# Performance work log

Hardware: AMD Instinct MI355X
Metric: run time of the kernel (lower is better)

The kernel has to match this reference:

```python
import jax, jax.numpy as jnp
import numpy as np

D = 2048      # in_features (model dim)
H = 1408      # d_intermediate (hidden per expert)
E = 16        # n_routed_experts
T = 16384     # flattened tokens
K = 4         # top_k experts per token


def setup_inputs() -> dict:
    key = jax.random.key(0)
    k1, k2, k3, k4, k5 = jax.random.split(key, 5)
    x = jax.random.normal(k1, (T, D), dtype=jnp.float32)
    weights = jax.random.uniform(k2, (T, K), dtype=jnp.float32)
    indices = jax.random.randint(k3, (T, K), 0, E)
    # Stacked GatedMLP params (bias=False as in mamba's GatedMLP):
    # fc1: [2H, D] per expert, fc2: [D, H] per expert
    W1 = jax.random.normal(k4, (E, 2 * H, D), dtype=jnp.float32) * (D ** -0.5)
    W2 = jax.random.normal(k5, (E, D, H), dtype=jnp.float32) * (H ** -0.5)
    return {"x": x, "weights": weights, "indices": indices, "W1": W1, "W2": W2}


def reference(x, weights, indices, W1, W2):
    # y[t] = sum_i ( GatedMLP_i(x[t]) * sum_k weights[t,k] * [indices[t,k]==i] )
    n_experts = W1.shape[0]
    y = jnp.zeros_like(x)
    for i in range(n_experts):  # small fixed expert loop
        # combined routing weight of expert i per token (handles duplicate hits like += in torch)
        cw = jnp.sum(weights * (indices == i), axis=-1)      # [T]
        h = x @ W1[i].T                                      # [T, 2H]
        u, g = jnp.split(h, 2, axis=-1)                      # chunk(2, dim=-1): (y, gate)
        out = (u * jax.nn.silu(g)) @ W2[i].T                 # [T, D]
        y = y + out * cw[:, None]
    return y
```

## Files before the change

kernel.cpp:

```cpp
#include <hip/hip_runtime.h>

#define D_ 2048
#define H_ 1408
#define E_ 16
#define T_ 16384
#define K_ 4
#define TK_ 65536
#define BM_ 256
#define BK_ 64
#define MAXT_ 272
#define CVTB_ 408

typedef __attribute__((ext_vector_type(8))) short bf16x8;
typedef __attribute__((ext_vector_type(4))) float f32x4;
typedef __attribute__((ext_vector_type(4))) unsigned short u16x4;

#define M_NT     49
#define M_TE     64
#define M_TR     (64 + MAXT_)
#define M_TN     (64 + 2*MAXT_)

#define XB_OFF   0ULL
#define W1B_OFF  67108864ULL
#define W2B_OFF  (W1B_OFF + 188743680ULL)
#define ACT_OFF  (W2B_OFF + 94371840ULL)
#define PERM_OFF (ACT_OFF + 184549376ULL)
#define WGT_OFF  (PERM_OFF + 262144ULL)
#define META_B   (WGT_OFF + 262144ULL)

#define SBAR()  __builtin_amdgcn_s_barrier()
#define SCHED() __builtin_amdgcn_sched_barrier(0)
#define LGK0()  asm volatile("s_waitcnt lgkmcnt(0)" ::: "memory")
#define LGK2()  asm volatile("s_waitcnt lgkmcnt(2)" ::: "memory")
#define LGK4()  asm volatile("s_waitcnt lgkmcnt(4)" ::: "memory")
#define LGK6()  asm volatile("s_waitcnt lgkmcnt(6)" ::: "memory")
#define VM6()   asm volatile("s_waitcnt vmcnt(6)" ::: "memory")
#define PRIO1() __builtin_amdgcn_s_setprio(1)
#define PRIO0() __builtin_amdgcn_s_setprio(0)

static __device__ __forceinline__ unsigned short f2bf(float f) {
  unsigned u = __builtin_bit_cast(unsigned, f);
  u += 0x7fffu + ((u >> 16) & 1u);
  return (unsigned short)(u >> 16);
}

static __device__ __forceinline__ void gload16(const void* g, unsigned ldsOff) {
  __builtin_amdgcn_global_load_lds(
      (const __attribute__((address_space(1))) unsigned int*)(unsigned long long)g,
      (__attribute__((address_space(3))) unsigned int*)(unsigned long long)ldsOff,
      16, 0, 0);
}

__global__ __launch_bounds__(1024) void prep_kernel(
    const float* __restrict__ x, const float* __restrict__ W1,
    const int* __restrict__ idx, const float* __restrict__ wts,
    float* __restrict__ y, unsigned short* __restrict__ xb,
    unsigned short* __restrict__ w1b, int* __restrict__ meta,
    int* __restrict__ perm, float* __restrict__ wgt) {
  const int tid = threadIdx.x;
  if (blockIdx.x == gridDim.x - 1) {
    __shared__ int cnt[E_], cur[E_];
    if (tid < E_) cnt[tid] = 0;
    __syncthreads();
    for (int i = tid; i < TK_; i += 1024) atomicAdd(&cnt[idx[i]], 1);
    __syncthreads();
    if (tid == 0) {
      int off = 0, nt = 0;
      for (int e = 0; e < E_; ++e) {
        cur[e] = off;
        const int c = cnt[e];
        for (int r = 0; r < c; r += BM_) {
          meta[M_TE + nt] = e;
          meta[M_TR + nt] = off + r;
          meta[M_TN + nt] = (c - r < BM_) ? (c - r) : BM_;
          ++nt;
        }
        off += c;
      }
      meta[M_NT] = nt;
    }
    __syncthreads();
    for (int i = tid; i < TK_; i += 1024) {
      const int pos = atomicAdd(&cur[idx[i]], 1);
      perm[pos] = i >> 2;
      wgt[pos] = wts[i];
    }
    return;
  }
  const long long base = ((long long)blockIdx.x * 1024 + tid) * 4;
  const long long stride = (long long)(gridDim.x - 1) * 1024 * 4;
  for (long long i = base; i < (long long)T_ * D_; i += stride)
    *reinterpret_cast<float4*>(y + i) = (float4){0.f, 0.f, 0.f, 0.f};
  for (long long i = base; i < (long long)T_ * D_; i += stride) {
    float4 v = *reinterpret_cast<const float4*>(x + i);
    u16x4 o = { f2bf(v.x), f2bf(v.y), f2bf(v.z), f2bf(v.w) };
    *reinterpret_cast<u16x4*>(xb + i) = o;
  }
  for (long long i = base; i < (long long)E_ * 2 * H_ * D_; i += stride) {
    float4 v = *reinterpret_cast<const float4*>(W1 + i);
    u16x4 o = { f2bf(v.x), f2bf(v.y), f2bf(v.z), f2bf(v.w) };
    *reinterpret_cast<u16x4*>(w1b + i) = o;
  }
}

__global__ __launch_bounds__(512, 2) void gemm1_kernel(
    const char* __restrict__ xb, const char* __restrict__ w1b,
    const int* __restrict__ perm, const int* __restrict__ meta,
    unsigned short* __restrict__ act,
    const float* __restrict__ W2, unsigned short* __restrict__ w2b) {
  const int tid = threadIdx.x;
  const int bid0 = (int)blockIdx.x;
  if (bid0 < CVTB_) {
    long long i = ((long long)bid0 * 512 + tid) * 4;
    const long long stride = (long long)CVTB_ * 512 * 4;
    for (; i < (long long)E_ * D_ * H_; i += stride) {
      float4 v = *reinterpret_cast<const float4*>(W2 + i);
      u16x4 o = { f2bf(v.x), f2bf(v.y), f2bf(v.z), f2bf(v.w) };
      *reinterpret_cast<u16x4*>(w2b + i) = o;
    }
    return;
  }
  __shared__ char lds[131072];
  int bid = bid0 - CVTB_;
  bid = (bid & 7) * 374 + (bid >> 3);
  const int tb = bid / 11;
  const int cb = bid - tb * 11;
  if (tb >= meta[M_NT]) return;
  const int e = meta[M_TE + tb];
  const int row0 = meta[M_TR + tb];
  const int nrows = meta[M_TN + tb];
  const int lane = tid & 63, wid = tid >> 6;
  const int wr = wid >> 2, wc = wid & 3;
  const unsigned ldsBase = (unsigned)(unsigned long long)&lds[0];
  constexpr int NT = D_ / BK_;

  const char* aSrc[4];
  const char* bSrc[4];
  {
    const int r8 = tid >> 3;
    const unsigned colb0 = (unsigned)(tid & 7) * 16u;
#pragma unroll
    for (int i = 0; i < 4; ++i) {
      const int r = r8 + i * 64;
      const unsigned colb = colb0 ^ ((unsigned)(r & 7) << 4);
      const int rc = (r < nrows) ? r : 0;
      aSrc[i] = xb + (size_t)perm[row0 + rc] * 4096 + colb;
      const int w1row = (i < 2) ? (cb * 128 + r) : (H_ + cb * 128 + (r - 128));
      bSrc[i] = w1b + (size_t)e * (2 * H_) * 4096ULL + (size_t)w1row * 4096 + colb;
    }
  }

  const int l15 = lane & 15, hi = lane >> 4;
  const unsigned swz = (unsigned)(l15 & 7) << 4;
  unsigned aOff[8], bOffU[2], bOffG[2];
#pragma unroll
  for (int m = 0; m < 8; ++m) {
    const int row = wr * 128 + m * 16 + l15;
    aOff[m] = (unsigned)(row * 128) + (((unsigned)hi * 16u) ^ swz);
  }
#pragma unroll
  for (int n = 0; n < 2; ++n) {
    const int ru = wc * 32 + n * 16 + l15;
    bOffU[n] = 65536u + (unsigned)(ru * 128) + (((unsigned)hi * 16u) ^ swz);
    const int rg = ru + 128;
    bOffG[n] = 65536u + (unsigned)(rg * 128) + (((unsigned)hi * 16u) ^ swz);
  }

  f32x4 aU[8][2], aG[8][2];
#pragma unroll
  for (int m = 0; m < 8; ++m)
#pragma unroll
    for (int n = 0; n < 2; ++n) {
      aU[m][n] = (f32x4){0.f, 0.f, 0.f, 0.f};
      aG[m][n] = (f32x4){0.f, 0.f, 0.f, 0.f};
    }

  auto STAGE_A = [&](int t, int h) {
    const int tt = (t < NT) ? t : (NT - 1);
    const size_t kb = (size_t)tt * 128;
    const unsigned dst = ldsBase + (unsigned)(t & 1) * 32768u + (unsigned)h * 16384u + (unsigned)tid * 16u;
    gload16(aSrc[h * 2 + 0] + kb, dst);
    gload16(aSrc[h * 2 + 1] + kb, dst + 8192u);
  };
  auto STAGE_B = [&](int t, int h) {
    const int tt = (t < NT) ? t : (NT - 1);
    const size_t kb = (size_t)tt * 128;
    const unsigned dst = ldsBase + 65536u + (unsigned)(t & 1) * 32768u + (unsigned)h * 16384u + (unsigned)tid * 16u;
    gload16(bSrc[h * 2 + 0] + kb, dst);
    gload16(bSrc[h * 2 + 1] + kb, dst + 8192u);
  };

  STAGE_B(0, 0); STAGE_B(0, 1); STAGE_A(0, 0); STAGE_A(0, 1);
  STAGE_B(1, 0); STAGE_B(1, 1); STAGE_A(1, 0);
  VM6(); SCHED(); SBAR();

  for (int t = 0; t < NT; ++t) {
    const char* base = lds + (unsigned)(t & 1) * 32768u;
    bf16x8 aLo[4][2], aHi[4][2], bu[2][2], bg[2][2];

#pragma unroll
    for (int ks = 0; ks < 2; ++ks) {
#pragma unroll
      for (int m = 0; m < 4; ++m)
        aLo[m][ks] = *reinterpret_cast<const bf16x8*>(base + (aOff[m] ^ (unsigned)(ks << 6)));
#pragma unroll
      for (int n = 0; n < 2; ++n)
        bu[n][ks] = *reinterpret_cast<const bf16x8*>(base + (bOffU[n] ^ (unsigned)(ks << 6)));
    }
    STAGE_A(t + 1, 1);
    LGK6(); SCHED();
    PRIO1();
#pragma unroll
    for (int m = 0; m < 4; ++m)
#pragma unroll
      for (int n = 0; n < 2; ++n)
        aU[m][n] = __builtin_amdgcn_mfma_f32_16x16x32_bf16(aLo[m][0], bu[n][0], aU[m][n], 0, 0, 0);
    LGK0(); SCHED();
#pragma unroll
    for (int m = 0; m < 4; ++m)
#pragma unroll
      for (int n = 0; n < 2; ++n)
        aU[m][n] = __builtin_amdgcn_mfma_f32_16x16x32_bf16(aLo[m][1], bu[n][1], aU[m][n], 0, 0, 0);
    PRIO0(); SCHED(); SBAR();

#pragma unroll
    for (int ks = 0; ks < 2; ++ks)
#pragma unroll
      for (int n = 0; n < 2; ++n)
        bg[n][ks] = *reinterpret_cast<const bf16x8*>(base + (bOffG[n] ^ (unsigned)(ks << 6)));
    STAGE_B(t + 2, 0);
    LGK2(); SCHED();
    PRIO1();
#pragma unroll
    for (int m = 0; m < 4; ++m)
#pragma unroll
      for (int n = 0; n < 2; ++n)
        aG[m][n] = __builtin_amdgcn_mfma_f32_16x16x32_bf16(aLo[m][0], bg[n][0], aG[m][n], 0, 0, 0);
    LGK0(); SCHED();
#pragma unroll
    for (int m = 0; m < 4; ++m)
#pragma unroll
      for (int n = 0; n < 2; ++n)
        aG[m][n] = __builtin_amdgcn_mfma_f32_16x16x32_bf16(aLo[m][1], bg[n][1], aG[m][n], 0, 0, 0);
    PRIO0(); SCHED(); SBAR();

#pragma unroll
    for (int ks = 0; ks < 2; ++ks)
#pragma unroll
      for (int m = 0; m < 4; ++m)
        aHi[m][ks] = *reinterpret_cast<const bf16x8*>(base + (aOff[4 + m] ^ (unsigned)(ks << 6)));
    STAGE_B(t + 2, 1);
    LGK4(); SCHED();
    PRIO1();
#pragma unroll
    for (int m = 0; m < 4; ++m)
#pragma unroll
      for (int n = 0; n < 2; ++n)
        aU[4 + m][n] = __builtin_amdgcn_mfma_f32_16x16x32_bf16(aHi[m][0], bu[n][0], aU[4 + m][n], 0, 0, 0);
    LGK0(); SCHED();
#pragma unroll
    for (int m = 0; m < 4; ++m)
#pragma unroll
      for (int n = 0; n < 2; ++n)
        aU[4 + m][n] = __builtin_amdgcn_mfma_f32_16x16x32_bf16(aHi[m][1], bu[n][1], aU[4 + m][n], 0, 0, 0);
    PRIO0(); SCHED(); SBAR();

    STAGE_A(t + 2, 0);
    VM6(); SCHED(); SBAR();
    PRIO1();
#pragma unroll
    for (int ks = 0; ks < 2; ++ks)
#pragma unroll
      for (int m = 0; m < 4; ++m)
#pragma unroll
        for (int n = 0; n < 2; ++n)
          aG[4 + m][n] = __builtin_amdgcn_mfma_f32_16x16x32_bf16(aHi[m][ks], bg[n][ks], aG[4 + m][n], 0, 0, 0);
    PRIO0(); SCHED();
  }

#pragma unroll
  for (int m = 0; m < 8; ++m)
#pragma unroll
    for (int j = 0; j < 4; ++j) {
      const int r = wr * 128 + m * 16 + hi * 4 + j;
      if (r < nrows) {
        const size_t rowBase = (size_t)(row0 + r) * H_ + (size_t)cb * 128 + (size_t)wc * 32;
#pragma unroll
        for (int n = 0; n < 2; ++n) {
          const float u = aU[m][n][j];
          const float g = aG[m][n][j];
          act[rowBase + n * 16 + l15] = f2bf(u * (g / (1.0f + __expf(-g))));
        }
      }
    }
}

__global__ __launch_bounds__(512, 2) void gemm2_kernel(
    const char* __restrict__ actb, const char* __restrict__ w2b,
    const int* __restrict__ perm, const float* __restrict__ wgt,
    const int* __restrict__ meta, float* __restrict__ y) {
  __shared__ char lds[131072];
  int bid = (int)blockIdx.x;
  bid = (bid & 7) * (int)(gridDim.x >> 3) + (bid >> 3);
  const int tb = bid >> 3;
  const int cb = bid & 7;
  if (tb >= meta[M_NT]) return;
  const int e = meta[M_TE + tb];
  const int row0 = meta[M_TR + tb];
  const int nrows = meta[M_TN + tb];
  const int tid = threadIdx.x, lane = tid & 63, wid = tid >> 6;
  const int wr = wid >> 2, wc = wid & 3;
  const unsigned ldsBase = (unsigned)(unsigned long long)&lds[0];
  constexpr int NT = H_ / BK_;

  const char* aSrc[4];
  const char* bSrc[4];
  {
    const int r8 = tid >> 3;
    const unsigned colb0 = (unsigned)(tid & 7) * 16u;
#pragma unroll
    for (int i = 0; i < 4; ++i) {
      const int r = r8 + i * 64;
      const unsigned colb = colb0 ^ ((unsigned)(r & 7) << 4);
      const int rc = (r < nrows) ? r : 0;
      aSrc[i] = actb + (size_t)(row0 + rc) * (H_ * 2) + colb;
      const int brow = cb * 256 + r;
      bSrc[i] = w2b + (size_t)e * D_ * (H_ * 2) + (size_t)brow * (H_ * 2) + colb;
    }
  }

  const int l15 = lane & 15, hi = lane >> 4;
  const unsigned swz = (unsigned)(l15 & 7) << 4;
  unsigned aOff[8], bOff[4];
#pragma unroll
  for (int m = 0; m < 8; ++m) {
    const int row = wr * 128 + m * 16 + l15;
    aOff[m] = (unsigned)(row * 128) + (((unsigned)hi * 16u) ^ swz);
  }
#pragma unroll
  for (int n = 0; n < 4; ++n) {
    const int rb = wc * 64 + n * 16 + l15;
    bOff[n] = 65536u + (unsigned)(rb * 128) + (((unsigned)hi * 16u) ^ swz);
  }

  f32x4 acc[8][4];
#pragma unroll
  for (int m = 0; m < 8; ++m)
#pragma unroll
    for (int n = 0; n < 4; ++n) acc[m][n] = (f32x4){0.f, 0.f, 0.f, 0.f};

  auto STAGE_A = [&](int t, int h) {
    const int tt = (t < NT) ? t : (NT - 1);
    const size_t kb = (size_t)tt * 128;
    const unsigned dst = ldsBase + (unsigned)(t & 1) * 32768u + (unsigned)h * 16384u + (unsigned)tid * 16u;
    gload16(aSrc[h * 2 + 0] + kb, dst);
    gload16(aSrc[h * 2 + 1] + kb, dst + 8192u);
  };
  auto STAGE_B = [&](int t, int h) {
    const int tt = (t < NT) ? t : (NT - 1);
    const size_t kb = (size_t)tt * 128;
    const unsigned dst = ldsBase + 65536u + (unsigned)(t & 1) * 32768u + (unsigned)h * 16384u + (unsigned)tid * 16u;
    gload16(bSrc[h * 2 + 0] + kb, dst);
    gload16(bSrc[h * 2 + 1] + kb, dst + 8192u);
  };

  STAGE_B(0, 0); STAGE_B(0, 1); STAGE_A(0, 0); STAGE_A(0, 1);
  STAGE_B(1, 0); STAGE_B(1, 1); STAGE_A(1, 0);
  VM6(); SCHED(); SBAR();

  for (int t = 0; t < NT; ++t) {
    const char* base = lds + (unsigned)(t & 1) * 32768u;
    bf16x8 aLo[4][2], aHi[4][2], b[4][2];

#pragma unroll
    for (int ks = 0; ks < 2; ++ks) {
#pragma unroll
      for (int m = 0; m < 4; ++m)
        aLo[m][ks] = *reinterpret_cast<const bf16x8*>(base + (aOff[m] ^ (unsigned)(ks << 6)));
#pragma unroll
      for (int n = 0; n < 2; ++n)
        b[n][ks] = *reinterpret_cast<const bf16x8*>(base + (bOff[n] ^ (unsigned)(ks << 6)));
    }
    STAGE_A(t + 1, 1);
    SCHED(); SBAR(); LGK6(); SCHED();
    PRIO1();
#pragma unroll
    for (int m = 0; m < 4; ++m)
#pragma unroll
      for (int n = 0; n < 2; ++n)
        acc[m][n] = __builtin_amdgcn_mfma_f32_16x16x32_bf16(aLo[m][0], b[n][0], acc[m][n], 0, 0, 0);
    LGK0(); SCHED();
#pragma unroll
    for (int m = 0; m < 4; ++m)
#pragma unroll
      for (int n = 0; n < 2; ++n)
        acc[m][n] = __builtin_amdgcn_mfma_f32_16x16x32_bf16(aLo[m][1], b[n][1], acc[m][n], 0, 0, 0);
    PRIO0(); SCHED(); SBAR();

#pragma unroll
    for (int ks = 0; ks < 2; ++ks)
#pragma unroll
      for (int n = 2; n < 4; ++n)
        b[n][ks] = *reinterpret_cast<const bf16x8*>(base + (bOff[n] ^ (unsigned)(ks << 6)));
    STAGE_B(t + 2, 0);
    SCHED(); SBAR(); LGK2(); SCHED();
    PRIO1();
#pragma unroll
    for (int m = 0; m < 4; ++m)
#pragma unroll
      for (int n = 2; n < 4; ++n)
        acc[m][n] = __builtin_amdgcn_mfma_f32_16x16x32_bf16(aLo[m][0], b[n][0], acc[m][n], 0, 0, 0);
    LGK0(); SCHED();
#pragma unroll
    for (int m = 0; m < 4; ++m)
#pragma unroll
      for (int n = 2; n < 4; ++n)
        acc[m][n] = __builtin_amdgcn_mfma_f32_16x16x32_bf16(aLo[m][1], b[n][1], acc[m][n], 0, 0, 0);
    PRIO0(); SCHED(); SBAR();

#pragma unroll
    for (int ks = 0; ks < 2; ++ks)
#pragma unroll
      for (int m = 0; m < 4; ++m)
        aHi[m][ks] = *reinterpret_cast<const bf16x8*>(base + (aOff[4 + m] ^ (unsigned)(ks << 6)));
    STAGE_B(t + 2, 1);
    SCHED(); SBAR(); LGK4(); SCHED();
    PRIO1();
#pragma unroll
    for (int m = 0; m < 4; ++m)
#pragma unroll
      for (int n = 0; n < 2; ++n)
        acc[4 + m][n] = __builtin_amdgcn_mfma_f32_16x16x32_bf16(aHi[m][0], b[n][0], acc[4 + m][n], 0, 0, 0);
    LGK0(); SCHED();
#pragma unroll
    for (int m = 0; m < 4; ++m)
#pragma unroll
      for (int n = 0; n < 2; ++n)
        acc[4 + m][n] = __builtin_amdgcn_mfma_f32_16x16x32_bf16(aHi[m][1], b[n][1], acc[4 + m][n], 0, 0, 0);
    PRIO0(); SCHED(); SBAR();

    STAGE_A(t + 2, 0);
    VM6(); SCHED(); SBAR();
    PRIO1();
#pragma unroll
    for (int ks = 0; ks < 2; ++ks)
#pragma unroll
      for (int m = 0; m < 4; ++m)
#pragma unroll
        for (int n = 2; n < 4; ++n)
          acc[4 + m][n] = __builtin_amdgcn_mfma_f32_16x16x32_bf16(aHi[m][ks], b[n][ks], acc[4 + m][n], 0, 0, 0);
    PRIO0(); SCHED(); SBAR();
  }

#pragma unroll
  for (int m = 0; m < 8; ++m)
#pragma unroll
    for (int j = 0; j < 4; ++j) {
      const int r = wr * 128 + m * 16 + hi * 4 + j;
      if (r < nrows) {
        const float w = wgt[row0 + r];
        const int token = perm[row0 + r];
        float* yrow = y + (size_t)token * D_ + (size_t)cb * 256 + (size_t)wc * 64;
#pragma unroll
        for (int n = 0; n < 4; ++n)
          unsafeAtomicAdd(&yrow[n * 16 + l15], acc[m][n][j] * w);
      }
    }
}

extern "C" void kernel_launch(void* const* d_in, const int* in_sizes, int n_in,
                              void* d_out, int out_size, void* d_ws, size_t ws_size,
                              hipStream_t stream) {
  const float* x   = (const float*)d_in[0];
  const float* wts = (const float*)d_in[1];
  const int*   idx = (const int*)d_in[2];
  const float* W1  = (const float*)d_in[3];
  const float* W2  = (const float*)d_in[4];
  float* y = (float*)d_out;
  char* ws = (char*)d_ws;

  unsigned short* xb  = (unsigned short*)(ws + XB_OFF);
  unsigned short* w1b = (unsigned short*)(ws + W1B_OFF);
  unsigned short* w2b = (unsigned short*)(ws + W2B_OFF);
  unsigned short* act = (unsigned short*)(ws + ACT_OFF);
  int*   perm = (int*)(ws + PERM_OFF);
  float* wgt  = (float*)(ws + WGT_OFF);
  int*   meta = (int*)(ws + META_B);

  prep_kernel<<<2049, 1024, 0, stream>>>(x, W1, idx, wts, y, xb, w1b, meta, perm, wgt);

  gemm1_kernel<<<CVTB_ + MAXT_ * (H_ / 128), 512, 0, stream>>>(
      (const char*)xb, (const char*)w1b, perm, meta, act, W2, w2b);

  gemm2_kernel<<<MAXT_ * (D_ / 256), 512, 0, stream>>>(
      (const char*)act, (const char*)w2b, perm, wgt, meta, y);
}
```

Measured before the change: 1.606 ms.

## Prefetch next tile's A-low and B-up fragments into registers during last MFMA phase

```diff
diff --git a/kernel.cpp b/kernel.cpp
--- a/kernel.cpp
+++ b/kernel.cpp
@@ -194,79 +194,79 @@
   STAGE_B(1, 0); STAGE_B(1, 1); STAGE_A(1, 0);
   VM6(); SCHED(); SBAR();
 
+  bf16x8 aLo[4][2], aHi[4][2], bu[2][2], bg[2][2];
+#pragma unroll
+  for (int ks = 0; ks < 2; ++ks) {
+#pragma unroll
+    for (int m = 0; m < 4; ++m)
+      aLo[m][ks] = *reinterpret_cast<const bf16x8*>(lds + (aOff[m] ^ (unsigned)(ks << 6)));
+#pragma unroll
+    for (int n = 0; n < 2; ++n)
+      bu[n][ks] = *reinterpret_cast<const bf16x8*>(lds + (bOffU[n] ^ (unsigned)(ks << 6)));
+  }
+
   for (int t = 0; t < NT; ++t) {
     const char* base = lds + (unsigned)(t & 1) * 32768u;
-    bf16x8 aLo[4][2], aHi[4][2], bu[2][2], bg[2][2];
-
-#pragma unroll
-    for (int ks = 0; ks < 2; ++ks) {
-#pragma unroll
-      for (int m = 0; m < 4; ++m)
-        aLo[m][ks] = *reinterpret_cast<const bf16x8*>(base + (aOff[m] ^ (unsigned)(ks << 6)));
-#pragma unroll
-      for (int n = 0; n < 2; ++n)
-        bu[n][ks] = *reinterpret_cast<const bf16x8*>(base + (bOffU[n] ^ (unsigned)(ks << 6)));
-    }
+    const char* nbase = lds + (unsigned)((t + 1) & 1) * 32768u;
+
+#pragma unroll
+    for (int ks = 0; ks < 2; ++ks)
+#pragma unroll
+      for (int n = 0; n < 2; ++n)
+        bg[n][ks] = *reinterpret_cast<const bf16x8*>(base + (bOffG[n] ^ (unsigned)(ks << 6)));
     STAGE_A(t + 1, 1);
-    LGK6(); SCHED();
-    PRIO1();
-#pragma unroll
-    for (int m = 0; m < 4; ++m)
-#pragma unroll
-      for (int n = 0; n < 2; ++n)
-        aU[m][n] = __builtin_amdgcn_mfma_f32_16x16x32_bf16(aLo[m][0], bu[n][0], aU[m][n], 0, 0, 0);
-    LGK0(); SCHED();
-#pragma unroll
-    for (int m = 0; m < 4; ++m)
-#pragma unroll
-      for (int n = 0; n < 2; ++n)
-        aU[m][n] = __builtin_amdgcn_mfma_f32_16x16x32_bf16(aLo[m][1], bu[n][1], aU[m][n], 0, 0, 0);
-    PRIO0(); SCHED(); SBAR();
-
-#pragma unroll
-    for (int ks = 0; ks < 2; ++ks)
-#pragma unroll
-      for (int n = 0; n < 2; ++n)
-        bg[n][ks] = *reinterpret_cast<const bf16x8*>(base + (bOffG[n] ^ (unsigned)(ks << 6)));
+    SCHED();
+    PRIO1();
+#pragma unroll
+    for (int ks = 0; ks < 2; ++ks)
+#pragma unroll
+      for (int m = 0; m < 4; ++m)
+#pragma unroll
+        for (int n = 0; n < 2; ++n)
+          aU[m][n] = __builtin_amdgcn_mfma_f32_16x16x32_bf16(aLo[m][ks], bu[n][ks], aU[m][n], 0, 0, 0);
+    PRIO0(); SCHED(); SBAR();
+
+#pragma unroll
+    for (int ks = 0; ks < 2; ++ks)
+#pragma unroll
+      for (int m = 0; m < 4; ++m)
+        aHi[m][ks] = *reinterpret_cast<const bf16x8*>(base + (aOff[4 + m] ^ (unsigned)(ks << 6)));
     STAGE_B(t + 2, 0);
-    LGK2(); SCHED();
-    PRIO1();
-#pragma unroll
-    for (int m = 0; m < 4; ++m)
-#pragma unroll
-      for (int n = 0; n < 2; ++n)
-        aG[m][n] = __builtin_amdgcn_mfma_f32_16x16x32_bf16(aLo[m][0], bg[n][0], aG[m][n], 0, 0, 0);
-    LGK0(); SCHED();
-#pragma unroll
-    for (int m = 0; m < 4; ++m)
-#pragma unroll
-      for (int n = 0; n < 2; ++n)
-        aG[m][n] = __builtin_amdgcn_mfma_f32_16x16x32_bf16(aLo[m][1], bg[n][1], aG[m][n], 0, 0, 0);
-    PRIO0(); SCHED(); SBAR();
-
-#pragma unroll
-    for (int ks = 0; ks < 2; ++ks)
-#pragma unroll
-      for (int m = 0; m < 4; ++m)
-        aHi[m][ks] = *reinterpret_cast<const bf16x8*>(base + (aOff[4 + m] ^ (unsigned)(ks << 6)));
+    SCHED();
+    PRIO1();
+#pragma unroll
+    for (int ks = 0; ks < 2; ++ks)
+#pragma unroll
+      for (int m = 0; m < 4; ++m)
+#pragma unroll
+        for (int n = 0; n < 2; ++n)
+          aG[m][n] = __builtin_amdgcn_mfma_f32_16x16x32_bf16(aLo[m][ks], bg[n][ks], aG[m][n], 0, 0, 0);
+    PRIO0(); SCHED(); SBAR();
+
     STAGE_B(t + 2, 1);
-    LGK4(); SCHED();
-    PRIO1();
-#pragma unroll
-    for (int m = 0; m < 4; ++m)
-#pragma unroll
-      for (int n = 0; n < 2; ++n)
-        aU[4 + m][n] = __builtin_amdgcn_mfma_f32_16x16x32_bf16(aHi[m][0], bu[n][0], aU[4 + m][n], 0, 0, 0);
-    LGK0(); SCHED();
-#pragma unroll
-    for (int m = 0; m < 4; ++m)
-#pragma unroll
-      for (int n = 0; n < 2; ++n)
-        aU[4 + m][n] = __builtin_amdgcn_mfma_f32_16x16x32_bf16(aHi[m][1], bu[n][1], aU[4 + m][n], 0, 0, 0);
+    SCHED();
+    PRIO1();
+#pragma unroll
+    for (int ks = 0; ks < 2; ++ks)
+#pragma unroll
+      for (int m = 0; m < 4; ++m)
+#pragma unroll
+        for (int n = 0; n < 2; ++n)
+          aU[4 + m][n] = __builtin_amdgcn_mfma_f32_16x16x32_bf16(aHi[m][ks], bu[n][ks], aU[4 + m][n], 0, 0, 0);
     PRIO0(); SCHED(); SBAR();
 
     STAGE_A(t + 2, 0);
     VM6(); SCHED(); SBAR();
+#pragma unroll
+    for (int ks = 0; ks < 2; ++ks) {
+#pragma unroll
+      for (int m = 0; m < 4; ++m)
+        aLo[m][ks] = *reinterpret_cast<const bf16x8*>(nbase + (aOff[m] ^ (unsigned)(ks << 6)));
+#pragma unroll
+      for (int n = 0; n < 2; ++n)
+        bu[n][ks] = *reinterpret_cast<const bf16x8*>(nbase + (bOffU[n] ^ (unsigned)(ks << 6)));
+    }
+    SCHED();
     PRIO1();
 #pragma unroll
     for (int ks = 0; ks < 2; ++ks)
```

Result: no change. 1.610 ms (+0.3%).
